# Kernel optimization log

Hardware: AMD Instinct MI355X
Metric: run time of the kernel (lower is better)

Reference implementation:

```python
import jax, jax.numpy as jnp
import numpy as np

K = 5
PAD = 2  # same-size output: pad = dilation*(k-1)/2


def _patches(x, k, pad):
    # x: [B, C, H, W] -> [B, C, k, k, H', W'] (matches torch F.unfold + view layout)
    B, C, H, W = x.shape
    p = jax.lax.conv_general_dilated_patches(
        x, (k, k), (1, 1), [(pad, pad), (pad, pad)])
    return p.reshape(B, C, k, k, p.shape[-2], p.shape[-1])


def setup_inputs() -> dict:
    key = jax.random.key(0)
    k1, k2, k3, k4 = jax.random.split(key, 4)
    B, Cin, Cout, Cg, H, W = 4, 32, 32, 8, 128, 128
    x = jax.random.normal(k1, (B, Cin, H, W), jnp.float32)
    guide = jax.random.normal(k2, (B, Cg, H, W), jnp.float32)
    weight = jax.random.normal(k3, (Cout, Cin, K, K), jnp.float32) * 0.05
    bias = jax.random.normal(k4, (Cout,), jnp.float32) * 0.05
    return {"x": x, "guide": guide, "weight": weight, "bias": bias}


def reference(x, guide, weight, bias):
    k = weight.shape[-1]
    # --- packernel2d (gaussian, smooth_kernel_type='none', channel_wise=False) ---
    gp = _patches(guide, k, PAD)                      # [B, Cg, k, k, H, W]
    center = gp[:, :, k // 2, k // 2][:, :, None, None]  # self-tap feature
    d = gp - center
    kernel = jnp.exp(-0.5 * jnp.sum(d * d, axis=1, keepdims=True))  # [B,1,k,k,H,W]
    # --- pacconv2d native path ---
    cols = _patches(x, k, PAD)                        # [B, Cin, k, k, H, W]
    out = jnp.einsum('bjklmn,ojkl->bomn', cols * kernel, weight)
    return out + bias[None, :, None, None]
```

## Files before the change

kernel.cpp:

```cpp
#include <hip/hip_runtime.h>

#define Bn   4
#define CIN  32
#define COUT 32
#define CG   8
#define Hh   128
#define Ww   128
#define KK   5
#define HW   (Hh * Ww)

#define TW   64
#define TH   4
#define PRW  68
#define PRH  8
#define NSLOT (PRW * PRH)

typedef _Float16 h8  __attribute__((ext_vector_type(8)));
typedef _Float16 h2  __attribute__((ext_vector_type(2)));
typedef float    f4  __attribute__((ext_vector_type(4)));

#define XOFF  0
#define XJG   8704
#define WOFF  34816
#define KOFF  60416
#define SMEMB 73216

#define XT_OFF 0
#define WT_OFF 4194304
#define GT_OFF 4245504
#define WS_NEED 5294080

__global__ __launch_bounds__(512) void prep(
    const float* __restrict__ x, const float* __restrict__ guide,
    const float* __restrict__ w,
    _Float16* __restrict__ xt, _Float16* __restrict__ wt, _Float16* __restrict__ gt)
{
    const int bid = blockIdx.x;
    const int tid = threadIdx.x;

    if (bid < 512) {
        const int b = bid >> 7, m = bid & 127;
        const int n = tid & 127, jh = tid >> 7;
        const float* xp = x + ((size_t)(b * CIN + jh * 8)) * HW + m * Ww + n;
        h8 v;
#pragma unroll
        for (int e = 0; e < 8; ++e) v[e] = (_Float16)xp[(size_t)e * HW];
        ((h8*)xt)[((size_t)b * HW + m * Ww + n) * 4 + jh] = v;
    } else if (bid < 562) {
        const int idx = (bid - 512) * 512 + tid;
        const int ht = idx >> 9;
        const int half = ht / 25, t = ht - half * 25;
        const int rem = idx & 511;
        const int jg = rem >> 7, o = (rem >> 3) & 15, e = rem & 7;
        wt[idx] = (_Float16)w[(size_t)(half * 16 + o) * (CIN * KK * KK) + (jg * 8 + e) * (KK * KK) + t];
    } else {
        const int gr = (bid - 562) * 4 + (tid >> 7);
        const int b = gr >> 7, m = gr & 127;
        const int n = tid & 127;
        const float* gp = guide + ((size_t)b * CG) * HW + m * Ww + n;
        h8 v;
#pragma unroll
        for (int e = 0; e < 8; ++e) v[e] = (_Float16)gp[(size_t)e * HW];
        ((h8*)gt)[(size_t)b * HW + m * Ww + n] = v;
    }
}

__global__ __launch_bounds__(512, 2) void pac_mfma7(
    const _Float16* __restrict__ xt, const _Float16* __restrict__ wt,
    const _Float16* __restrict__ gt, const float* __restrict__ bias,
    float* __restrict__ out)
{
    __shared__ __align__(16) unsigned char smem[SMEMB];

    const int tid = threadIdx.x;
    const int bx  = blockIdx.x;
    const int bz  = blockIdx.y;
    const int tm = (bx >> 1) * TH;
    const int tn = (bx & 1) * TW;

    const int lane = tid & 63;
    const int l15 = lane & 15, kg = lane >> 4;

    const h8* wh1 = (const h8*)wt + 1600;
    h8 B1r[25];
#pragma unroll
    for (int t = 0; t < 25; ++t)
        B1r[t] = wh1[t * 64 + kg * 16 + l15];

    const int pxbase = bz * HW;
#pragma unroll
    for (int it = 0; it < 5; ++it) {
        const int idx = it * 512 + tid;
        if (idx < 2176) {
            const int slot = idx >> 2, jg = idx & 3;
            const int r = slot / PRW;
            const int c = slot - r * PRW;
            const int gm = tm + r - 2, gn = tn + c - 2;
            h8 v = {};
            if ((unsigned)gm < (unsigned)Hh && (unsigned)gn < (unsigned)Ww)
                v = *(const h8*)(xt + ((size_t)(pxbase + gm * Ww + gn)) * 32 + jg * 8);
            *(h8*)(smem + XOFF + jg * XJG + slot * 16) = v;
        }
    }

    const h8* wth = (const h8*)wt;
#pragma unroll
    for (int it = 0; it < 4; ++it) {
        const int idx = it * 512 + tid;
        if (idx < 1600)
            *(h8*)(smem + WOFF + idx * 16) = wth[idx];
    }

    {
        const int px = tid & 255, th = tid >> 8;
        const int pr = px >> 6, pc = px & 63;
        const int pg = px >> 5, ps = (px >> 4) & 1, pi = px & 15;
        const int m = tm + pr, n = tn + pc;
        const h8* gtb = (const h8*)gt + (size_t)bz * HW;
        const h8 c8 = gtb[m * Ww + n];
        float cg[8];
#pragma unroll
        for (int i = 0; i < 8; ++i) cg[i] = (float)c8[i];
        int t = 0;
#pragma unroll
        for (int k = 0; k < KK; ++k) {
#pragma unroll
            for (int l = 0; l < KK; ++l) {
                if ((t < 13) == (th == 0)) {
                    const int gm = m + k - 2, gn = n + l - 2;
                    h8 gv = {};
                    if ((unsigned)gm < (unsigned)Hh && (unsigned)gn < (unsigned)Ww)
                        gv = gtb[gm * Ww + gn];
                    float ss = 0.f;
#pragma unroll
                    for (int i = 0; i < 8; ++i) {
                        const float d = (float)gv[i] - cg[i];
                        ss = fmaf(d, d, ss);
                    }
                    *(_Float16*)(smem + KOFF + t * 512 + ((pg * 16 + pi) * 2 + ps) * 2) =
                        (_Float16)__expf(-0.5f * ss);
                }
                ++t;
            }
        }
    }

    __syncthreads();

    const int wv = tid >> 6;
    const int st0 = wv * 32, st1 = st0 + 16;
    const int r0 = wv >> 1;
    const int c00 = (wv & 1) * 32;

    f4 acc00 = {0.f,0.f,0.f,0.f}, acc01 = {0.f,0.f,0.f,0.f};
    f4 acc10 = {0.f,0.f,0.f,0.f}, acc11 = {0.f,0.f,0.f,0.f};
    const unsigned char* xg = smem + XOFF + kg * XJG;
    const int kbase = KOFF + (wv * 16 + l15) * 4;

    int t = 0;
#pragma unroll
    for (int k = 0; k < KK; ++k) {
#pragma unroll
        for (int l = 0; l < KK; ++l) {
            const int abase = ((r0 + k) * PRW + c00 + l + l15) * 16;
            h8 A0 = *(const h8*)(xg + abase);
            h8 A1 = *(const h8*)(xg + abase + 256);
            h8 B0 = *(const h8*)(smem + WOFF + t * 1024 + kg * 256 + l15 * 16);
            h2 kk = *(const h2*)(smem + kbase + t * 512);

            h8 A0s = A0 * kk[0];
            h8 A1s = A1 * kk[1];

            acc00 = __builtin_amdgcn_mfma_f32_16x16x32_f16(A0s, B0,     acc00, 0, 0, 0);
            acc01 = __builtin_amdgcn_mfma_f32_16x16x32_f16(A0s, B1r[t], acc01, 0, 0, 0);
            acc10 = __builtin_amdgcn_mfma_f32_16x16x32_f16(A1s, B0,     acc10, 0, 0, 0);
            acc11 = __builtin_amdgcn_mfma_f32_16x16x32_f16(A1s, B1r[t], acc11, 0, 0, 0);
            ++t;
        }
    }

    const float bv0 = bias[l15], bv1 = bias[16 + l15];
#pragma unroll
    for (int i = 0; i < 4; ++i) {
        acc00[i] += bv0; acc10[i] += bv0;
        acc01[i] += bv1; acc11[i] += bv1;
    }

    __syncthreads();
    float* outst = (float*)smem;
    *(f4*)(outst + l15 * 260 + st0 + kg * 4) = acc00;
    *(f4*)(outst + l15 * 260 + st1 + kg * 4) = acc10;
    *(f4*)(outst + (16 + l15) * 260 + st0 + kg * 4) = acc01;
    *(f4*)(outst + (16 + l15) * 260 + st1 + kg * 4) = acc11;
    __syncthreads();

    const int o = tid >> 4;
    const int i = tid & 15;
    float* op = out + ((size_t)(bz * COUT + o)) * HW;
#pragma unroll
    for (int c = 0; c < 4; ++c) {
        f4 v = *(const f4*)(outst + o * 260 + c * 64 + i * 4);
        *(f4*)(op + (size_t)(tm + c) * Ww + tn + i * 4) = v;
    }
}

typedef _Float16 h4v __attribute__((ext_vector_type(4)));
__global__ __launch_bounds__(512, 4) void pac_mfma2(
    const float* __restrict__ x, const float* __restrict__ guide,
    const float* __restrict__ weight, const float* __restrict__ bias,
    float* __restrict__ out)
{
    __shared__ __align__(16) unsigned char smem[SMEMB];
    const int tid  = threadIdx.x;
    const int bx   = blockIdx.x;
    const int half = blockIdx.y;
    const int bz   = blockIdx.z;
    const int tm = (bx >> 1) * TH;
    const int tn = (bx & 1) * TW;

    const float* xb = x + (size_t)bz * CIN * HW;
#pragma unroll
    for (int it = 0; it < 34; ++it) {
        const int idx  = it * 512 + tid;
        const int j    = idx / NSLOT;
        const int slot = idx - j * NSLOT;
        const int r    = slot / PRW;
        const int c    = slot - r * PRW;
        const int gm = tm + r - 2, gn = tn + c - 2;
        float v = 0.f;
        if ((unsigned)gm < (unsigned)Hh && (unsigned)gn < (unsigned)Ww)
            v = xb[(size_t)j * HW + gm * Ww + gn];
        *(_Float16*)(smem + XOFF + (j >> 3) * XJG + slot * 16 + (j & 7) * 2) = (_Float16)v;
    }
#pragma unroll
    for (int it = 0; it < 25; ++it) {
        const int idx = it * 512 + tid;
        const int o = idx & 15;
        const int j = (idx >> 4) & 31;
        const int t = idx >> 9;
        const float v = weight[(size_t)(half * 16 + o) * (CIN * KK * KK) + j * (KK * KK) + t];
        *(_Float16*)(smem + WOFF + t * 1024 + (j >> 3) * 256 + o * 16 + (j & 7) * 2) = (_Float16)v;
    }
    {
        const int px = tid & 255, th = tid >> 8;
        const int pr = px >> 6, pc = px & 63;
        const int m = tm + pr, n = tn + pc;
        const float* gb = guide + ((size_t)bz * CG) * HW + m * Ww + n;
        float center[CG];
#pragma unroll
        for (int c = 0; c < CG; ++c) center[c] = gb[c * HW];
        int t = 0;
#pragma unroll
        for (int k = 0; k < KK; ++k) {
            const int dm = k - 2;
            const bool rowok = ((unsigned)(m + dm) < (unsigned)Hh);
#pragma unroll
            for (int l = 0; l < KK; ++l) {
                if ((t < 13) == (th == 0)) {
                    const int dn = l - 2;
                    const bool ok = rowok && ((unsigned)(n + dn) < (unsigned)Ww);
                    float ss = 0.f;
#pragma unroll
                    for (int c = 0; c < CG; ++c) {
                        float gv = ok ? gb[c * HW + dm * Ww + dn] : 0.f;
                        float d = gv - center[c];
                        ss = fmaf(d, d, ss);
                    }
                    *(_Float16*)(smem + KOFF + t * 512 + px * 2) = (_Float16)__expf(-0.5f * ss);
                }
                ++t;
            }
        }
    }
    __syncthreads();
    const int lane = tid & 63;
    const int l15 = lane & 15, kg = lane >> 4;
    const int wv = tid >> 6;
    const int st0 = wv * 32, st1 = st0 + 16;
    const int r0 = wv >> 1;
    const int c00 = (wv & 1) * 32;
    f4 acc0 = {0.f, 0.f, 0.f, 0.f}, acc1 = {0.f, 0.f, 0.f, 0.f};
    const unsigned char* xg = smem + XOFF + kg * XJG;
    const float bv = bias[half * 16 + l15];
    int t = 0;
#pragma unroll
    for (int k = 0; k < KK; ++k) {
#pragma unroll
        for (int l = 0; l < KK; ++l) {
            const int abase = ((r0 + k) * PRW + c00 + l + l15) * 16;
            h8 A0 = *(const h8*)(xg + abase);
            h8 A1 = *(const h8*)(xg + abase + 256);
            h8 Bv = *(const h8*)(smem + WOFF + t * 1024 + kg * 256 + l15 * 16);
            f4 p0 = __builtin_amdgcn_mfma_f32_16x16x32_f16(A0, Bv, (f4){0.f,0.f,0.f,0.f}, 0, 0, 0);
            f4 p1 = __builtin_amdgcn_mfma_f32_16x16x32_f16(A1, Bv, (f4){0.f,0.f,0.f,0.f}, 0, 0, 0);
            h4v k0 = *(const h4v*)(smem + KOFF + t * 512 + (st0 + kg * 4) * 2);
            h4v k1 = *(const h4v*)(smem + KOFF + t * 512 + (st1 + kg * 4) * 2);
#pragma unroll
            for (int i = 0; i < 4; ++i) {
                acc0[i] = fmaf((float)k0[i], p0[i], acc0[i]);
                acc1[i] = fmaf((float)k1[i], p1[i], acc1[i]);
            }
            ++t;
        }
    }
#pragma unroll
    for (int i = 0; i < 4; ++i) { acc0[i] += bv; acc1[i] += bv; }
    __syncthreads();
    float* outst = (float*)smem;
    *(f4*)(outst + l15 * 260 + st0 + kg * 4) = acc0;
    *(f4*)(outst + l15 * 260 + st1 + kg * 4) = acc1;
    __syncthreads();
    const int o = tid >> 5;
    const int p = (tid & 31) * 8;
    f4 v0 = *(const f4*)(outst + o * 260 + p);
    f4 v1 = *(const f4*)(outst + o * 260 + p + 4);
    const int mr = p >> 6, nc = p & 63;
    float* op = out + ((size_t)(bz * COUT + half * 16 + o)) * HW + (size_t)(tm + mr) * Ww + tn + nc;
    *(f4*)op = v0;
    *(f4*)(op + 4) = v1;
}

extern "C" void kernel_launch(void* const* d_in, const int* in_sizes, int n_in,
                              void* d_out, int out_size, void* d_ws, size_t ws_size,
                              hipStream_t stream) {
    const float* x      = (const float*)d_in[0];
    const float* guide  = (const float*)d_in[1];
    const float* weight = (const float*)d_in[2];
    const float* bias   = (const float*)d_in[3];
    float* out = (float*)d_out;

    if (ws_size >= (size_t)WS_NEED) {
        _Float16* xt = (_Float16*)((char*)d_ws + XT_OFF);
        _Float16* wt = (_Float16*)((char*)d_ws + WT_OFF);
        _Float16* gt = (_Float16*)((char*)d_ws + GT_OFF);
        prep<<<dim3(690), 512, 0, stream>>>(x, guide, weight, xt, wt, gt);
        pac_mfma7<<<dim3(64, Bn), 512, 0, stream>>>(xt, wt, gt, bias, out);
    } else {
        pac_mfma2<<<dim3(64, 2, Bn), 512, 0, stream>>>(x, guide, weight, bias, out);
    }
}
```

Measured before the change: 23.28 us.

## Halve spatial tile, drop weight LDS staging, read weights from global/L1

The main kernel now uses 256-thread blocks over 64x2 output tiles, doubling the grid to 512 blocks, with about 32 KB of LDS per block to allow higher occupancy. Weights are no longer staged in shared memory or held in 25 preloaded registers. Each MFMA step instead reads both weight halves straight from global memory, relying on L1/L2 caching. The aim is to cut per-block setup, LDS and register pressure and to spread work across more CUs, at the cost of a larger relative halo overhead (6 rows loaded for 2 output rows) and repeated global weight loads inside the inner loop.

```diff
diff --git a/kernel.cpp b/kernel.cpp
--- a/kernel.cpp
+++ b/kernel.cpp
@@ -15,6 +15,12 @@
 #define PRH  8
 #define NSLOT (PRW * PRH)
 
+#define T3W  64
+#define T3H  2
+#define P3W  68
+#define P3H  6
+#define N3SLOT (P3W * P3H)
+
 typedef _Float16 h8  __attribute__((ext_vector_type(8)));
 typedef _Float16 h2  __attribute__((ext_vector_type(2)));
 typedef float    f4  __attribute__((ext_vector_type(4)));
@@ -24,6 +30,10 @@
 #define WOFF  34816
 #define KOFF  60416
 #define SMEMB 73216
+
+#define X3JG  6560
+#define K3OFF 26240
+#define SMEM3 32640
 
 #define XT_OFF 0
 #define WT_OFF 4194304
@@ -65,54 +75,39 @@
     }
 }
 
-__global__ __launch_bounds__(512, 2) void pac_mfma7(
+__global__ __launch_bounds__(256, 4) void pac_mfma8(
     const _Float16* __restrict__ xt, const _Float16* __restrict__ wt,
     const _Float16* __restrict__ gt, const float* __restrict__ bias,
     float* __restrict__ out)
 {
-    __shared__ __align__(16) unsigned char smem[SMEMB];
+    __shared__ __align__(16) unsigned char smem[SMEM3];
 
     const int tid = threadIdx.x;
     const int bx  = blockIdx.x;
     const int bz  = blockIdx.y;
-    const int tm = (bx >> 1) * TH;
-    const int tn = (bx & 1) * TW;
+    const int tm = (bx >> 1) * T3H;
+    const int tn = (bx & 1) * T3W;
 
     const int lane = tid & 63;
     const int l15 = lane & 15, kg = lane >> 4;
 
-    const h8* wh1 = (const h8*)wt + 1600;
-    h8 B1r[25];
-#pragma unroll
-    for (int t = 0; t < 25; ++t)
-        B1r[t] = wh1[t * 64 + kg * 16 + l15];
-
     const int pxbase = bz * HW;
 #pragma unroll
-    for (int it = 0; it < 5; ++it) {
-        const int idx = it * 512 + tid;
-        if (idx < 2176) {
+    for (int it = 0; it < 7; ++it) {
+        const int idx = it * 256 + tid;
+        if (idx < 1632) {
             const int slot = idx >> 2, jg = idx & 3;
-            const int r = slot / PRW;
-            const int c = slot - r * PRW;
+            const int r = slot / P3W, c = slot - r * P3W;
             const int gm = tm + r - 2, gn = tn + c - 2;
             h8 v = {};
             if ((unsigned)gm < (unsigned)Hh && (unsigned)gn < (unsigned)Ww)
                 v = *(const h8*)(xt + ((size_t)(pxbase + gm * Ww + gn)) * 32 + jg * 8);
-            *(h8*)(smem + XOFF + jg * XJG + slot * 16) = v;
-        }
-    }
-
-    const h8* wth = (const h8*)wt;
-#pragma unroll
-    for (int it = 0; it < 4; ++it) {
-        const int idx = it * 512 + tid;
-        if (idx < 1600)
-            *(h8*)(smem + WOFF + idx * 16) = wth[idx];
+            *(h8*)(smem + jg * X3JG + slot * 16) = v;
+        }
     }
 
     {
-        const int px = tid & 255, th = tid >> 8;
+        const int px = tid & 127, th = tid >> 7;
         const int pr = px >> 6, pc = px & 63;
         const int pg = px >> 5, ps = (px >> 4) & 1, pi = px & 15;
         const int m = tm + pr, n = tn + pc;
@@ -137,7 +132,7 @@
                         const float d = (float)gv[i] - cg[i];
                         ss = fmaf(d, d, ss);
                     }
-                    *(_Float16*)(smem + KOFF + t * 512 + ((pg * 16 + pi) * 2 + ps) * 2) =
+                    *(_Float16*)(smem + K3OFF + t * 256 + (pg * 64 + pi * 4 + ps * 2)) =
                         (_Float16)__expf(-0.5f * ss);
                 }
                 ++t;
@@ -154,27 +149,30 @@
 
     f4 acc00 = {0.f,0.f,0.f,0.f}, acc01 = {0.f,0.f,0.f,0.f};
     f4 acc10 = {0.f,0.f,0.f,0.f}, acc11 = {0.f,0.f,0.f,0.f};
-    const unsigned char* xg = smem + XOFF + kg * XJG;
-    const int kbase = KOFF + (wv * 16 + l15) * 4;
+    const unsigned char* xg = smem + kg * X3JG;
+    const int kbase = K3OFF + wv * 64 + l15 * 4;
+    const h8* wb0 = (const h8*)wt + kg * 16 + l15;
+    const h8* wb1 = wb0 + 1600;
 
     int t = 0;
 #pragma unroll
     for (int k = 0; k < KK; ++k) {
 #pragma unroll
         for (int l = 0; l < KK; ++l) {
-            const int abase = ((r0 + k) * PRW + c00 + l + l15) * 16;
+            const int abase = ((r0 + k) * P3W + c00 + l + l15) * 16;
             h8 A0 = *(const h8*)(xg + abase);
             h8 A1 = *(const h8*)(xg + abase + 256);
-            h8 B0 = *(const h8*)(smem + WOFF + t * 1024 + kg * 256 + l15 * 16);
-            h2 kk = *(const h2*)(smem + kbase + t * 512);
+            h8 B0 = wb0[t * 64];
+            h8 B1 = wb1[t * 64];
+            h2 kk = *(const h2*)(smem + kbase + t * 256);
 
             h8 A0s = A0 * kk[0];
             h8 A1s = A1 * kk[1];
 
-            acc00 = __builtin_amdgcn_mfma_f32_16x16x32_f16(A0s, B0,     acc00, 0, 0, 0);
-            acc01 = __builtin_amdgcn_mfma_f32_16x16x32_f16(A0s, B1r[t], acc01, 0, 0, 0);
-            acc10 = __builtin_amdgcn_mfma_f32_16x16x32_f16(A1s, B0,     acc10, 0, 0, 0);
-            acc11 = __builtin_amdgcn_mfma_f32_16x16x32_f16(A1s, B1r[t], acc11, 0, 0, 0);
+            acc00 = __builtin_amdgcn_mfma_f32_16x16x32_f16(A0s, B0, acc00, 0, 0, 0);
+            acc01 = __builtin_amdgcn_mfma_f32_16x16x32_f16(A0s, B1, acc01, 0, 0, 0);
+            acc10 = __builtin_amdgcn_mfma_f32_16x16x32_f16(A1s, B0, acc10, 0, 0, 0);
+            acc11 = __builtin_amdgcn_mfma_f32_16x16x32_f16(A1s, B1, acc11, 0, 0, 0);
             ++t;
         }
     }
@@ -188,20 +186,21 @@
 
     __syncthreads();
     float* outst = (float*)smem;
-    *(f4*)(outst + l15 * 260 + st0 + kg * 4) = acc00;
-    *(f4*)(outst + l15 * 260 + st1 + kg * 4) = acc10;
-    *(f4*)(outst + (16 + l15) * 260 + st0 + kg * 4) = acc01;
-    *(f4*)(outst + (16 + l15) * 260 + st1 + kg * 4) = acc11;
-    __syncthreads();
-
-    const int o = tid >> 4;
-    const int i = tid & 15;
-    float* op = out + ((size_t)(bz * COUT + o)) * HW;
-#pragma unroll
-    for (int c = 0; c < 4; ++c) {
-        f4 v = *(const f4*)(outst + o * 260 + c * 64 + i * 4);
-        *(f4*)(op + (size_t)(tm + c) * Ww + tn + i * 4) = v;
-    }
+    *(f4*)(outst + l15 * 132 + st0 + kg * 4) = acc00;
+    *(f4*)(outst + l15 * 132 + st1 + kg * 4) = acc10;
+    *(f4*)(outst + (16 + l15) * 132 + st0 + kg * 4) = acc01;
+    *(f4*)(outst + (16 + l15) * 132 + st1 + kg * 4) = acc11;
+    __syncthreads();
+
+    const int o = tid >> 3;
+    const int i = tid & 7;
+    const int px0 = i * 16;
+    const int row = px0 >> 6, col = px0 & 63;
+    float* op = out + ((size_t)(bz * COUT + o)) * HW + (size_t)(tm + row) * Ww + tn + col;
+    const float* src = outst + o * 132 + px0;
+#pragma unroll
+    for (int c = 0; c < 4; ++c)
+        *(f4*)(op + c * 4) = *(const f4*)(src + c * 4);
 }
 
 typedef _Float16 h4v __attribute__((ext_vector_type(4)));
@@ -334,7 +333,7 @@
         _Float16* wt = (_Float16*)((char*)d_ws + WT_OFF);
         _Float16* gt = (_Float16*)((char*)d_ws + GT_OFF);
         prep<<<dim3(690), 512, 0, stream>>>(x, guide, weight, xt, wt, gt);
-        pac_mfma7<<<dim3(64, Bn), 512, 0, stream>>>(xt, wt, gt, bias, out);
+        pac_mfma8<<<dim3(128, Bn), 256, 0, stream>>>(xt, wt, gt, bias, out);
     } else {
         pac_mfma2<<<dim3(64, 2, Bn), 512, 0, stream>>>(x, guide, weight, bias, out);
     }
```

Measured after the change: 26.58 us. 14.2% more time.

## Pre-pad x halo in workspace and stage tiles via direct global-to-LDS loads

Applied to the files above, without the earlier changes.

The prep kernel now writes x into a zero-padded 132x132 layout and adds blocks that zero the border, so the main kernel no longer needs bounds checks when loading the halo tile. The main kernel then stages the x tile and the weights into shared memory with global_load_lds, which copies straight from global memory to LDS and skips the register round trip. The intent is to cut load instructions and VGPR pressure in the staging phase. The trade-offs are a larger workspace, extra prep blocks, and reliance on the LDS layout matching the per-wave 1KB chunking that global_load_lds produces.

```diff
diff --git a/kernel.cpp b/kernel.cpp
--- a/kernel.cpp
+++ b/kernel.cpp
@@ -15,6 +15,8 @@
 #define PRH  8
 #define NSLOT (PRW * PRH)
 
+#define PADW 132
+
 typedef _Float16 h8  __attribute__((ext_vector_type(8)));
 typedef _Float16 h2  __attribute__((ext_vector_type(2)));
 typedef float    f4  __attribute__((ext_vector_type(4)));
@@ -26,9 +28,13 @@
 #define SMEMB 73216
 
 #define XT_OFF 0
-#define WT_OFF 4194304
-#define GT_OFF 4245504
-#define WS_NEED 5294080
+#define WT_OFF 4460544
+#define GT_OFF 4511744
+#define WS_NEED 5560320
+
+#define GLDS(gp, lp) __builtin_amdgcn_global_load_lds( \
+    (const __attribute__((address_space(1))) void*)(gp), \
+    (__attribute__((address_space(3))) void*)(lp), 16, 0, 0)
 
 __global__ __launch_bounds__(512) void prep(
     const float* __restrict__ x, const float* __restrict__ guide,
@@ -45,7 +51,7 @@
         h8 v;
 #pragma unroll
         for (int e = 0; e < 8; ++e) v[e] = (_Float16)xp[(size_t)e * HW];
-        ((h8*)xt)[((size_t)b * HW + m * Ww + n) * 4 + jh] = v;
+        ((h8*)xt)[(((size_t)b * PADW + m + 2) * PADW + n + 2) * 4 + jh] = v;
     } else if (bid < 562) {
         const int idx = (bid - 512) * 512 + tid;
         const int ht = idx >> 9;
@@ -53,7 +59,7 @@
         const int rem = idx & 511;
         const int jg = rem >> 7, o = (rem >> 3) & 15, e = rem & 7;
         wt[idx] = (_Float16)w[(size_t)(half * 16 + o) * (CIN * KK * KK) + (jg * 8 + e) * (KK * KK) + t];
-    } else {
+    } else if (bid < 690) {
         const int gr = (bid - 562) * 4 + (tid >> 7);
         const int b = gr >> 7, m = gr & 127;
         const int n = tid & 127;
@@ -62,10 +68,29 @@
 #pragma unroll
         for (int e = 0; e < 8; ++e) v[e] = (_Float16)gp[(size_t)e * HW];
         ((h8*)gt)[(size_t)b * HW + m * Ww + n] = v;
+    } else {
+        const int idx = (bid - 690) * 512 + tid;
+        if (idx < 4160) {
+            const int b = idx / 1040, r = idx - b * 1040;
+            int mp, np;
+            if (r < 528) {
+                const int mr = r / 132;
+                mp = (mr < 2) ? mr : mr + 128;
+                np = r - mr * 132;
+            } else {
+                const int r2 = r - 528;
+                mp = 2 + (r2 >> 2);
+                const int q = r2 & 3;
+                np = (q < 2) ? q : q + 128;
+            }
+            h8 z = {};
+            h8* dst = (h8*)xt + (((size_t)b * PADW + mp) * PADW + np) * 4;
+            dst[0] = z; dst[1] = z; dst[2] = z; dst[3] = z;
+        }
     }
 }
 
-__global__ __launch_bounds__(512, 2) void pac_mfma7(
+__global__ __launch_bounds__(512, 2) void pac_mfma10(
     const _Float16* __restrict__ xt, const _Float16* __restrict__ wt,
     const _Float16* __restrict__ gt, const float* __restrict__ bias,
     float* __restrict__ out)
@@ -80,36 +105,28 @@
 
     const int lane = tid & 63;
     const int l15 = lane & 15, kg = lane >> 4;
+    const int wv = tid >> 6;
+
+    for (int c = wv; c < 34; c += 8) {
+        const int i = c * 64 + lane;
+        const int jg = i / NSLOT;
+        const int slot = i - jg * NSLOT;
+        const int r = slot / PRW, cc = slot - r * PRW;
+        const _Float16* g = xt +
+            ((((size_t)bz * PADW + tm + r) * PADW + tn + cc) * 4 + jg) * 8;
+        GLDS(g, smem + XOFF + c * 1024);
+    }
+
+    for (int c = wv; c < 25; c += 8) {
+        const _Float16* g = wt + (c * 64 + lane) * 8;
+        GLDS(g, smem + WOFF + c * 1024);
+    }
 
     const h8* wh1 = (const h8*)wt + 1600;
     h8 B1r[25];
 #pragma unroll
     for (int t = 0; t < 25; ++t)
         B1r[t] = wh1[t * 64 + kg * 16 + l15];
-
-    const int pxbase = bz * HW;
-#pragma unroll
-    for (int it = 0; it < 5; ++it) {
-        const int idx = it * 512 + tid;
-        if (idx < 2176) {
-            const int slot = idx >> 2, jg = idx & 3;
-            const int r = slot / PRW;
-            const int c = slot - r * PRW;
-            const int gm = tm + r - 2, gn = tn + c - 2;
-            h8 v = {};
-            if ((unsigned)gm < (unsigned)Hh && (unsigned)gn < (unsigned)Ww)
-                v = *(const h8*)(xt + ((size_t)(pxbase + gm * Ww + gn)) * 32 + jg * 8);
-            *(h8*)(smem + XOFF + jg * XJG + slot * 16) = v;
-        }
-    }
-
-    const h8* wth = (const h8*)wt;
-#pragma unroll
-    for (int it = 0; it < 4; ++it) {
-        const int idx = it * 512 + tid;
-        if (idx < 1600)
-            *(h8*)(smem + WOFF + idx * 16) = wth[idx];
-    }
 
     {
         const int px = tid & 255, th = tid >> 8;
@@ -147,7 +164,6 @@
 
     __syncthreads();
 
-    const int wv = tid >> 6;
     const int st0 = wv * 32, st1 = st0 + 16;
     const int r0 = wv >> 1;
     const int c00 = (wv & 1) * 32;
@@ -333,8 +349,8 @@
         _Float16* xt = (_Float16*)((char*)d_ws + XT_OFF);
         _Float16* wt = (_Float16*)((char*)d_ws + WT_OFF);
         _Float16* gt = (_Float16*)((char*)d_ws + GT_OFF);
-        prep<<<dim3(690), 512, 0, stream>>>(x, guide, weight, xt, wt, gt);
-        pac_mfma7<<<dim3(64, Bn), 512, 0, stream>>>(xt, wt, gt, bias, out);
+        prep<<<dim3(699), 512, 0, stream>>>(x, guide, weight, xt, wt, gt);
+        pac_mfma10<<<dim3(64, Bn), 512, 0, stream>>>(xt, wt, gt, bias, out);
     } else {
         pac_mfma2<<<dim3(64, 2, Bn), 512, 0, stream>>>(x, guide, weight, bias, out);
     }
```

Measured after the change: 23.57 us. No clear change (+1.2%).
